# Kernel optimization log

Hardware: AMD Instinct MI355X
Metric: run time of the kernel (lower is better)

## Reference

```python
import jax, jax.numpy as jnp
import numpy as np

ND, NG, E = 25000, 20000, 1_000_000
DIN_D, DIN_G, H, OUT = 128, 128, 128, 128


def setup_inputs() -> dict:
    key = jax.random.key(0)
    ks = jax.random.split(key, 12)

    def w(k, i, o):
        return jax.random.normal(k, (i, o), jnp.float32) / np.float32(np.sqrt(i))

    return {
        "x_disease": jax.random.normal(ks[0], (ND, DIN_D), jnp.float32),
        "x_gene": jax.random.normal(ks[1], (NG, DIN_G), jnp.float32),
        "src": jax.random.randint(ks[2], (E,), 0, ND, dtype=jnp.int32),  # disease endpoint
        "dst": jax.random.randint(ks[3], (E,), 0, NG, dtype=jnp.int32),  # gene endpoint
        # layer 1, relation disease->gene: lin_l acts on aggregated disease feats, lin_r on gene feats
        "w1_dg_l": w(ks[4], DIN_D, H), "b1_dg": jnp.zeros((H,), jnp.float32), "w1_dg_r": w(ks[5], DIN_G, H),
        # layer 1, relation gene->disease (reverse edges)
        "w1_gd_l": w(ks[6], DIN_G, H), "b1_gd": jnp.zeros((H,), jnp.float32), "w1_gd_r": w(ks[7], DIN_D, H),
        # layer 2
        "w2_dg_l": w(ks[8], H, OUT), "b2_dg": jnp.zeros((OUT,), jnp.float32), "w2_dg_r": w(ks[9], H, OUT),
        "w2_gd_l": w(ks[10], H, OUT), "b2_gd": jnp.zeros((OUT,), jnp.float32), "w2_gd_r": w(ks[11], H, OUT),
    }


def _sage(x_src, x_dst, e_src, e_dst, n_dst, W_l, b_l, W_r):
    """Bipartite SAGEConv: lin_l(mean of source neighbors) + lin_r(x_dst)."""
    msg = x_src[e_src]                                         # [E, d] gather
    s = jax.ops.segment_sum(msg, e_dst, num_segments=n_dst)    # [n_dst, d]
    cnt = jax.ops.segment_sum(jnp.ones((e_dst.shape[0],), x_src.dtype),
                              e_dst, num_segments=n_dst)
    mean = s / jnp.maximum(cnt, 1.0)[:, None]                  # isolated nodes -> 0
    return mean @ W_l + b_l + x_dst @ W_r


def reference(x_disease, x_gene, src, dst,
              w1_dg_l, b1_dg, w1_dg_r, w1_gd_l, b1_gd, w1_gd_r,
              w2_dg_l, b2_dg, w2_dg_r, w2_gd_l, b2_gd, w2_gd_r):
    # HeteroConv aggr='sum': each node type receives from exactly one relation here,
    # so the cross-relation sum is the single relation output.
    g1 = _sage(x_disease, x_gene, src, dst, NG, w1_dg_l, b1_dg, w1_dg_r)   # gene <- disease
    d1 = _sage(x_gene, x_disease, dst, src, ND, w1_gd_l, b1_gd, w1_gd_r)   # disease <- gene (rev)
    g2 = _sage(d1, g1, src, dst, NG, w2_dg_l, b2_dg, w2_dg_r)
    d2 = _sage(g1, d1, dst, src, ND, w2_gd_l, b2_gd, w2_gd_r)
    return d2, g2
```

## Files before the change

### kernel.cpp

```cpp
#include <hip/hip_runtime.h>
#include <hip/hip_fp16.h>

#define ND 25000
#define NG 20000
#define NTOT (ND + NG)
#define NSCAN_BLOCKS 44
#define NBLK 128

typedef _Float16 half8 __attribute__((ext_vector_type(8)));
typedef float f32x4 __attribute__((ext_vector_type(4)));
typedef float f32x2 __attribute__((ext_vector_type(2)));

#define OFF_CNT    0ull
#define OFF_ROW    180224ull
#define OFF_BSUM   360448ull
#define OFF_PARTD  360704ull
#define OFF_PARTG  6760704ull
#define OFF_COL    11880704ull
#define OFF_WSW    15880704ull
#define OFF_XDH    16142848ull
#define OFF_XGH    22542848ull
#define OFF_X8D    27662848ull
#define OFF_X8G    30862848ull
#define OFF_MDH    33422848ull
#define OFF_MGH    39822848ull
#define OFF_D1H    44942848ull
#define OFF_G1H    51342848ull
#define OFF_D18    56462848ull
#define OFF_G18    59662848ull

struct WPtrs { const float* w[8]; };

__global__ __launch_bounds__(256) void prep(const float* __restrict__ xd,
                                            const float* __restrict__ xg,
                                            __half* __restrict__ yd,
                                            __half* __restrict__ yg,
                                            unsigned char* __restrict__ y8d,
                                            unsigned char* __restrict__ y8g,
                                            WPtrs p, _Float16* __restrict__ wsw) {
    int t = threadIdx.x;
    if (blockIdx.x < 8) {
        int mat = blockIdx.x;
        const float* W = p.w[mat];
        _Float16* o = wsw + (size_t)mat * 16384;
        for (int rep = 0; rep < 8; ++rep) {
            int slot = rep * 256 + t;
            int lane = slot & 63, grp = slot >> 6;
            int kc = grp & 3, ntile = grp >> 2;
            int nn = ntile * 16 + (lane & 15);
            int kb = kc * 32 + (lane >> 4) * 8;
            half8 v;
#pragma unroll
            for (int j = 0; j < 8; ++j) v[j] = (_Float16)W[(size_t)(kb + j) * 128 + nn];
            *(half8*)(o + (size_t)slot * 8) = v;
        }
        return;
    }
    const int ndq = ND * 32;
    const int tot = ndq + NG * 32;
    int i = (blockIdx.x - 8) * 256 + t;
    if (i >= tot) return;
    const float* x;
    __half* y;
    unsigned char* y8;
    int idx;
    if (i < ndq) { x = xd; y = yd; y8 = y8d; idx = i; }
    else         { x = xg; y = yg; y8 = y8g; idx = i - ndq; }
    float4 v = ((const float4*)x)[idx];
    ((__half2*)y)[idx * 2 + 0] = __floats2half2_rn(v.x, v.y);
    ((__half2*)y)[idx * 2 + 1] = __floats2half2_rn(v.z, v.w);
    int p8 = __builtin_amdgcn_cvt_pk_fp8_f32(v.x, v.y, 0, false);
    p8 = __builtin_amdgcn_cvt_pk_fp8_f32(v.z, v.w, p8, true);
    ((int*)y8)[idx] = p8;
}

__global__ __launch_bounds__(256) void hist2(const int* __restrict__ src,
                                             const int* __restrict__ dst,
                                             unsigned short* __restrict__ partD,
                                             unsigned short* __restrict__ partG, int E) {
    __shared__ unsigned int h[12544];
    int t = threadIdx.x, b = blockIdx.x;
    bool isD = b < NBLK;
    int bb = isD ? b : b - NBLK;
    const int* key = isD ? src : dst;
    int nw = isD ? (ND / 2) : (NG / 2);
    for (int i = t; i < nw; i += 256) h[i] = 0;
    __syncthreads();
    int e0 = (int)(((long long)E * bb) / NBLK);
    int e1 = (int)(((long long)E * (bb + 1)) / NBLK);
    for (int e = e0 + t; e < e1; e += 256) {
        int k = key[e];
        atomicAdd(&h[k >> 1], 1u << ((k & 1) * 16));
    }
    __syncthreads();
    unsigned int* po = (unsigned int*)((isD ? partD : partG) + (size_t)bb * (isD ? ND : NG));
    for (int i = t; i < nw; i += 256) po[i] = h[i];
}

__global__ __launch_bounds__(256) void colscan2(unsigned short* __restrict__ partD,
                                                unsigned short* __restrict__ partG,
                                                int* __restrict__ cnt) {
    int k = blockIdx.x * 256 + threadIdx.x;
    if (k >= NTOT) return;
    unsigned short* part;
    int nb, kk;
    if (k < ND) { part = partD; nb = ND; kk = k; }
    else        { part = partG; nb = NG; kk = k - ND; }
    int run = 0;
#pragma unroll 8
    for (int b = 0; b < NBLK; ++b) {
        size_t idx = (size_t)b * nb + kk;
        int v = part[idx];
        part[idx] = (unsigned short)run;
        run += v;
    }
    cnt[k] = run;
}

__global__ __launch_bounds__(256) void scan1(const int* __restrict__ cnt,
                                             int* __restrict__ row,
                                             int* __restrict__ bsum, int N) {
    __shared__ int sd[256];
    int t = threadIdx.x;
    int base = blockIdx.x * 1024 + t * 4;
    int v[4];
#pragma unroll
    for (int j = 0; j < 4; ++j) {
        int idx = base + j;
        v[j] = (idx < N) ? cnt[idx] : 0;
    }
    int tsum = v[0] + v[1] + v[2] + v[3];
    sd[t] = tsum;
    __syncthreads();
    for (int off = 1; off < 256; off <<= 1) {
        int x = (t >= off) ? sd[t - off] : 0;
        __syncthreads();
        sd[t] += x;
        __syncthreads();
    }
    int run = sd[t] - tsum;
#pragma unroll
    for (int j = 0; j < 4; ++j) {
        int idx = base + j;
        if (idx < N) row[idx] = run;
        run += v[j];
    }
    if (t == 255) bsum[blockIdx.x] = sd[255];
}

__global__ __launch_bounds__(256) void scan2(int* __restrict__ row,
                                             const int* __restrict__ bsum,
                                             int N, int total) {
    int off = 0;
    for (int b2 = 0; b2 < (int)blockIdx.x; ++b2) off += bsum[b2];
    int t = threadIdx.x;
    int base = blockIdx.x * 1024 + t * 4;
#pragma unroll
    for (int j = 0; j < 4; ++j) {
        int idx = base + j;
        if (idx < N) row[idx] += off;
    }
    if (blockIdx.x == 0 && t == 0) row[N] = total;
}

__global__ __launch_bounds__(256) void fill2(const int* __restrict__ src,
                                             const int* __restrict__ dst,
                                             const int* __restrict__ row,
                                             const unsigned short* __restrict__ partD,
                                             const unsigned short* __restrict__ partG,
                                             unsigned short* __restrict__ col, int E) {
    __shared__ unsigned int h[12544];
    int t = threadIdx.x, b = blockIdx.x;
    bool isD = b < NBLK;
    int bb = isD ? b : b - NBLK;
    const int* key = isD ? src : dst;
    const int* val = isD ? dst : src;
    const int* rowp = isD ? row : row + ND;
    int nw = isD ? (ND / 2) : (NG / 2);
    const unsigned int* pi =
        (const unsigned int*)((isD ? partD : partG) + (size_t)bb * (isD ? ND : NG));
    for (int i = t; i < nw; i += 256) h[i] = pi[i];
    __syncthreads();
    int e0 = (int)(((long long)E * bb) / NBLK);
    int e1 = (int)(((long long)E * (bb + 1)) / NBLK);
    for (int e = e0 + t; e < e1; e += 256) {
        int k = key[e];
        int v = val[e];
        unsigned int old = atomicAdd(&h[k >> 1], 1u << ((k & 1) * 16));
        int rank = (old >> ((k & 1) * 16)) & 0xffff;
        col[rowp[k] + rank] = (unsigned short)v;
    }
}

__global__ __launch_bounds__(256) void agg8m(const unsigned char* __restrict__ Xg,
                                             const unsigned char* __restrict__ Xd,
                                             const int* __restrict__ row,
                                             const unsigned short* __restrict__ col,
                                             __half* __restrict__ outd,
                                             __half* __restrict__ outg) {
    int wid = threadIdx.x >> 6, lane = threadIdx.x & 63;
    int node = blockIdx.x * 4 + wid;
    if (node >= NTOT) return;
    const unsigned char* X;
    _Float16* out;
    int nloc;
    if (node < ND) { X = Xg; out = (_Float16*)outd; nloc = node; }
    else           { X = Xd; out = (_Float16*)outg; nloc = node - ND; }
    int b = row[node], e = row[node + 1];
    int g = lane >> 3, f = lane & 7;
    float acc[16];
#pragma unroll
    for (int k = 0; k < 16; ++k) acc[k] = 0.f;
    int j = b + g;
    for (; j + 8 < e; j += 16) {
        int c0 = col[j], c1 = col[j + 8];
        int4 w0 = *(const int4*)(X + (size_t)c0 * 128 + f * 16);
        int4 w1 = *(const int4*)(X + (size_t)c1 * 128 + f * 16);
        const int* wa = (const int*)&w0;
        const int* wb = (const int*)&w1;
#pragma unroll
        for (int q = 0; q < 4; ++q) {
            f32x2 l0 = __builtin_amdgcn_cvt_pk_f32_fp8(wa[q], false);
            f32x2 h0 = __builtin_amdgcn_cvt_pk_f32_fp8(wa[q], true);
            f32x2 l1 = __builtin_amdgcn_cvt_pk_f32_fp8(wb[q], false);
            f32x2 h1 = __builtin_amdgcn_cvt_pk_f32_fp8(wb[q], true);
            acc[q * 4 + 0] += l0[0] + l1[0];
            acc[q * 4 + 1] += l0[1] + l1[1];
            acc[q * 4 + 2] += h0[0] + h1[0];
            acc[q * 4 + 3] += h0[1] + h1[1];
        }
    }
    if (j < e) {
        int c = col[j];
        int4 w = *(const int4*)(X + (size_t)c * 128 + f * 16);
        const int* wa = (const int*)&w;
#pragma unroll
        for (int q = 0; q < 4; ++q) {
            f32x2 l = __builtin_amdgcn_cvt_pk_f32_fp8(wa[q], false);
            f32x2 h = __builtin_amdgcn_cvt_pk_f32_fp8(wa[q], true);
            acc[q * 4 + 0] += l[0];
            acc[q * 4 + 1] += l[1];
            acc[q * 4 + 2] += h[0];
            acc[q * 4 + 3] += h[1];
        }
    }
#pragma unroll
    for (int k = 0; k < 16; ++k) {
        acc[k] += __shfl_xor(acc[k], 8, 64);
        acc[k] += __shfl_xor(acc[k], 16, 64);
        acc[k] += __shfl_xor(acc[k], 32, 64);
    }
    if (g == 0) {
        int deg = e - b;
        float r = 1.0f / (float)(deg > 0 ? deg : 1);
        half8 o0, o1;
#pragma unroll
        for (int k = 0; k < 8; ++k) o0[k] = (_Float16)(acc[k] * r);
#pragma unroll
        for (int k = 0; k < 8; ++k) o1[k] = (_Float16)(acc[8 + k] * r);
        _Float16* op = out + (size_t)nloc * 128 + f * 16;
        *(half8*)op = o0;
        *(half8*)(op + 8) = o1;
    }
}

struct GemmDual {
    const __half *A1d, *A2d, *A1g, *A2g;
    const _Float16 *W1d, *W2d, *W1g, *W2g;
    const float *biasd, *biasg;
    float *Yfd, *Yfg;
    __half *Yhd, *Yhg;
    unsigned char *Y8d, *Y8g;
};
__global__ __launch_bounds__(256) void gemm2(GemmDual p, int nblkD) {
    int bx = blockIdx.x;
    const __half *A1, *A2;
    const _Float16 *W1, *W2;
    const float* bias;
    float* Yf;
    __half* Yh;
    unsigned char* Y8;
    int n, b0;
    if (bx < nblkD) {
        A1 = p.A1d; A2 = p.A2d; W1 = p.W1d; W2 = p.W2d; bias = p.biasd;
        Yf = p.Yfd; Yh = p.Yhd; Y8 = p.Y8d; n = ND; b0 = bx;
    } else {
        A1 = p.A1g; A2 = p.A2g; W1 = p.W1g; W2 = p.W2g; bias = p.biasg;
        Yf = p.Yfg; Yh = p.Yhg; Y8 = p.Y8g; n = NG; b0 = bx - nblkD;
    }
    int t = threadIdx.x;
    int wave = t >> 6, lane = t & 63;
    int row0 = b0 * 64 + wave * 16;
    if (row0 >= n) return;
    int m = lane & 15, quad = lane >> 4;
    int arow = row0 + m;
    if (arow >= n) arow = n - 1;
    const _Float16* a1p = (const _Float16*)A1 + (size_t)arow * 128 + quad * 8;
    const _Float16* a2p = (const _Float16*)A2 + (size_t)arow * 128 + quad * 8;
    half8 a1[4], a2[4];
#pragma unroll
    for (int kc = 0; kc < 4; ++kc) {
        a1[kc] = *(const half8*)(a1p + kc * 32);
        a2[kc] = *(const half8*)(a2p + kc * 32);
    }
#pragma unroll
    for (int ntile = 0; ntile < 8; ++ntile) {
        f32x4 acc = {0.f, 0.f, 0.f, 0.f};
#pragma unroll
        for (int kc = 0; kc < 4; ++kc) {
            half8 b1 = *(const half8*)(W1 + (size_t)((ntile * 4 + kc) * 64 + lane) * 8);
            acc = __builtin_amdgcn_mfma_f32_16x16x32_f16(a1[kc], b1, acc, 0, 0, 0);
            half8 b2 = *(const half8*)(W2 + (size_t)((ntile * 4 + kc) * 64 + lane) * 8);
            acc = __builtin_amdgcn_mfma_f32_16x16x32_f16(a2[kc], b2, acc, 0, 0, 0);
        }
        int colx = ntile * 16 + m;
        float bb = bias[colx];
#pragma unroll
        for (int r = 0; r < 4; ++r) {
            int rr = row0 + quad * 4 + r;
            if (rr < n) {
                float v = acc[r] + bb;
                if (Yf) {
                    Yf[(size_t)rr * 128 + colx] = v;
                } else {
                    Yh[(size_t)rr * 128 + colx] = __float2half(v);
                    int p8 = __builtin_amdgcn_cvt_pk_fp8_f32(v, v, 0, false);
                    Y8[(size_t)rr * 128 + colx] = (unsigned char)(p8 & 0xff);
                }
            }
        }
    }
}

extern "C" void kernel_launch(void* const* d_in, const int* in_sizes, int n_in,
                              void* d_out, int out_size, void* d_ws, size_t ws_size,
                              hipStream_t stream) {
    const float* x_d     = (const float*)d_in[0];
    const float* x_g     = (const float*)d_in[1];
    const int*   src     = (const int*)d_in[2];
    const int*   dst     = (const int*)d_in[3];
    const float* w1_dg_l = (const float*)d_in[4];
    const float* b1_dg   = (const float*)d_in[5];
    const float* w1_dg_r = (const float*)d_in[6];
    const float* w1_gd_l = (const float*)d_in[7];
    const float* b1_gd   = (const float*)d_in[8];
    const float* w1_gd_r = (const float*)d_in[9];
    const float* w2_dg_l = (const float*)d_in[10];
    const float* b2_dg   = (const float*)d_in[11];
    const float* w2_dg_r = (const float*)d_in[12];
    const float* w2_gd_l = (const float*)d_in[13];
    const float* b2_gd   = (const float*)d_in[14];
    const float* w2_gd_r = (const float*)d_in[15];
    float* out = (float*)d_out;

    char* ws = (char*)d_ws;
    int*            cnt   = (int*)(ws + OFF_CNT);
    int*            row   = (int*)(ws + OFF_ROW);
    int*            bsum  = (int*)(ws + OFF_BSUM);
    unsigned short* partD = (unsigned short*)(ws + OFF_PARTD);
    unsigned short* partG = (unsigned short*)(ws + OFF_PARTG);
    unsigned short* col   = (unsigned short*)(ws + OFF_COL);
    _Float16*       wsw   = (_Float16*)(ws + OFF_WSW);
    __half*         xd_h  = (__half*)(ws + OFF_XDH);
    __half*         xg_h  = (__half*)(ws + OFF_XGH);
    unsigned char*  x8d   = (unsigned char*)(ws + OFF_X8D);
    unsigned char*  x8g   = (unsigned char*)(ws + OFF_X8G);
    __half*         md_h  = (__half*)(ws + OFF_MDH);
    __half*         mg_h  = (__half*)(ws + OFF_MGH);
    __half*         d1_h  = (__half*)(ws + OFF_D1H);
    __half*         g1_h  = (__half*)(ws + OFF_G1H);
    unsigned char*  d1_8  = (unsigned char*)(ws + OFF_D18);
    unsigned char*  g1_8  = (unsigned char*)(ws + OFF_G18);

    const int E = in_sizes[2];
    const int nblkD = (ND + 63) / 64;
    const int nblkG = (NG + 63) / 64;

    WPtrs wp;
    wp.w[0] = w1_dg_l; wp.w[1] = w1_dg_r; wp.w[2] = w1_gd_l; wp.w[3] = w1_gd_r;
    wp.w[4] = w2_dg_l; wp.w[5] = w2_dg_r; wp.w[6] = w2_gd_l; wp.w[7] = w2_gd_r;
    prep<<<8 + (NTOT * 32 + 255) / 256, 256, 0, stream>>>(x_d, x_g, xd_h, xg_h, x8d, x8g, wp, wsw);

    hist2<<<2 * NBLK, 256, 0, stream>>>(src, dst, partD, partG, E);
    colscan2<<<(NTOT + 255) / 256, 256, 0, stream>>>(partD, partG, cnt);
    scan1<<<NSCAN_BLOCKS, 256, 0, stream>>>(cnt, row, bsum, NTOT);
    scan2<<<NSCAN_BLOCKS, 256, 0, stream>>>(row, bsum, NTOT, 2 * E);
    fill2<<<2 * NBLK, 256, 0, stream>>>(src, dst, row, partD, partG, col, E);

    agg8m<<<(NTOT + 3) / 4, 256, 0, stream>>>(x8g, x8d, row, col, md_h, mg_h);
    GemmDual g1p;
    g1p.A1d = md_h; g1p.A2d = xd_h; g1p.W1d = wsw + 2 * 16384; g1p.W2d = wsw + 3 * 16384;
    g1p.biasd = b1_gd; g1p.Yfd = nullptr; g1p.Yhd = d1_h; g1p.Y8d = d1_8;
    g1p.A1g = mg_h; g1p.A2g = xg_h; g1p.W1g = wsw + 0 * 16384; g1p.W2g = wsw + 1 * 16384;
    g1p.biasg = b1_dg; g1p.Yfg = nullptr; g1p.Yhg = g1_h; g1p.Y8g = g1_8;
    gemm2<<<nblkD + nblkG, 256, 0, stream>>>(g1p, nblkD);

    agg8m<<<(NTOT + 3) / 4, 256, 0, stream>>>(g1_8, d1_8, row, col, md_h, mg_h);
    GemmDual g2p;
    g2p.A1d = md_h; g2p.A2d = d1_h; g2p.W1d = wsw + 6 * 16384; g2p.W2d = wsw + 7 * 16384;
    g2p.biasd = b2_gd; g2p.Yfd = out; g2p.Yhd = nullptr; g2p.Y8d = nullptr;
    g2p.A1g = mg_h; g2p.A2g = g1_h; g2p.W1g = wsw + 4 * 16384; g2p.W2g = wsw + 5 * 16384;
    g2p.biasg = b2_dg; g2p.Yfg = out + (size_t)ND * 128; g2p.Yhg = nullptr; g2p.Y8g = nullptr;
    gemm2<<<nblkD + nblkG, 256, 0, stream>>>(g2p, nblkD);
}
```

Before: 255.7 us.

## Fuse aggregation into GEMM via LDS, merge prep with histogram, single-block scan

Mean aggregation now runs inside the GEMM kernel. Each wave gathers and averages 16 node rows into LDS, then feeds them straight into the MFMA, so the fp16 mean buffers are no longer written to and re-read from global memory. Weight/feature prep and the edge histogram share one launch. The two-pass scan becomes a single 1024-thread block. Launches and global traffic drop, but each GEMM block now serializes 16 gathers per wave, and there are far fewer waves in flight for hiding gather latency.

```diff
diff --git a/kernel.cpp b/kernel.cpp
--- a/kernel.cpp
+++ b/kernel.cpp
@@ -4,8 +4,9 @@
 #define ND 25000
 #define NG 20000
 #define NTOT (ND + NG)
-#define NSCAN_BLOCKS 44
 #define NBLK 128
+#define PREPB 1024
+#define LDP 136
 
 typedef _Float16 half8 __attribute__((ext_vector_type(8)));
 typedef float f32x4 __attribute__((ext_vector_type(4)));
@@ -13,7 +14,6 @@
 
 #define OFF_CNT    0ull
 #define OFF_ROW    180224ull
-#define OFF_BSUM   360448ull
 #define OFF_PARTD  360704ull
 #define OFF_PARTG  6760704ull
 #define OFF_COL    11880704ull
@@ -22,27 +22,48 @@
 #define OFF_XGH    22542848ull
 #define OFF_X8D    27662848ull
 #define OFF_X8G    30862848ull
-#define OFF_MDH    33422848ull
-#define OFF_MGH    39822848ull
-#define OFF_D1H    44942848ull
-#define OFF_G1H    51342848ull
-#define OFF_D18    56462848ull
-#define OFF_G18    59662848ull
+#define OFF_D1H    33422848ull
+#define OFF_G1H    39822848ull
+#define OFF_D18    44942848ull
+#define OFF_G18    48142848ull
 
 struct WPtrs { const float* w[8]; };
 
-__global__ __launch_bounds__(256) void prep(const float* __restrict__ xd,
-                                            const float* __restrict__ xg,
-                                            __half* __restrict__ yd,
-                                            __half* __restrict__ yg,
-                                            unsigned char* __restrict__ y8d,
-                                            unsigned char* __restrict__ y8g,
-                                            WPtrs p, _Float16* __restrict__ wsw) {
-    int t = threadIdx.x;
-    if (blockIdx.x < 8) {
-        int mat = blockIdx.x;
-        const float* W = p.w[mat];
-        _Float16* o = wsw + (size_t)mat * 16384;
+__global__ __launch_bounds__(256) void prep_hist(const float* __restrict__ xd,
+                                                 const float* __restrict__ xg,
+                                                 __half* __restrict__ ydh,
+                                                 __half* __restrict__ ygh,
+                                                 unsigned char* __restrict__ y8d,
+                                                 unsigned char* __restrict__ y8g,
+                                                 WPtrs wp, _Float16* __restrict__ wsw,
+                                                 const int* __restrict__ src,
+                                                 const int* __restrict__ dst,
+                                                 unsigned short* __restrict__ partD,
+                                                 unsigned short* __restrict__ partG, int E) {
+    __shared__ unsigned int h[12544];
+    int bx = blockIdx.x, t = threadIdx.x;
+    if (bx < 2 * NBLK) {
+        bool isD = bx < NBLK;
+        int bb = isD ? bx : bx - NBLK;
+        const int* key = isD ? src : dst;
+        int nw = isD ? (ND / 2) : (NG / 2);
+        for (int i = t; i < nw; i += 256) h[i] = 0;
+        __syncthreads();
+        int e0 = (int)(((long long)E * bb) / NBLK);
+        int e1 = (int)(((long long)E * (bb + 1)) / NBLK);
+        for (int e = e0 + t; e < e1; e += 256) {
+            int k = key[e];
+            atomicAdd(&h[k >> 1], 1u << ((k & 1) * 16));
+        }
+        __syncthreads();
+        unsigned int* po = (unsigned int*)((isD ? partD : partG) + (size_t)bb * (isD ? ND : NG));
+        for (int i = t; i < nw; i += 256) po[i] = h[i];
+        return;
+    }
+    int pb = bx - 2 * NBLK;
+    if (pb < 8) {
+        const float* W = wp.w[pb];
+        _Float16* o = wsw + (size_t)pb * 16384;
         for (int rep = 0; rep < 8; ++rep) {
             int slot = rep * 256 + t;
             int lane = slot & 63, grp = slot >> 6;
@@ -54,47 +75,23 @@
             for (int j = 0; j < 8; ++j) v[j] = (_Float16)W[(size_t)(kb + j) * 128 + nn];
             *(half8*)(o + (size_t)slot * 8) = v;
         }
-        return;
     }
     const int ndq = ND * 32;
     const int tot = ndq + NG * 32;
-    int i = (blockIdx.x - 8) * 256 + t;
-    if (i >= tot) return;
-    const float* x;
-    __half* y;
-    unsigned char* y8;
-    int idx;
-    if (i < ndq) { x = xd; y = yd; y8 = y8d; idx = i; }
-    else         { x = xg; y = yg; y8 = y8g; idx = i - ndq; }
-    float4 v = ((const float4*)x)[idx];
-    ((__half2*)y)[idx * 2 + 0] = __floats2half2_rn(v.x, v.y);
-    ((__half2*)y)[idx * 2 + 1] = __floats2half2_rn(v.z, v.w);
-    int p8 = __builtin_amdgcn_cvt_pk_fp8_f32(v.x, v.y, 0, false);
-    p8 = __builtin_amdgcn_cvt_pk_fp8_f32(v.z, v.w, p8, true);
-    ((int*)y8)[idx] = p8;
-}
-
-__global__ __launch_bounds__(256) void hist2(const int* __restrict__ src,
-                                             const int* __restrict__ dst,
-                                             unsigned short* __restrict__ partD,
-                                             unsigned short* __restrict__ partG, int E) {
-    __shared__ unsigned int h[12544];
-    int t = threadIdx.x, b = blockIdx.x;
-    bool isD = b < NBLK;
-    int bb = isD ? b : b - NBLK;
-    const int* key = isD ? src : dst;
-    int nw = isD ? (ND / 2) : (NG / 2);
-    for (int i = t; i < nw; i += 256) h[i] = 0;
-    __syncthreads();
-    int e0 = (int)(((long long)E * bb) / NBLK);
-    int e1 = (int)(((long long)E * (bb + 1)) / NBLK);
-    for (int e = e0 + t; e < e1; e += 256) {
-        int k = key[e];
-        atomicAdd(&h[k >> 1], 1u << ((k & 1) * 16));
-    }
-    __syncthreads();
-    unsigned int* po = (unsigned int*)((isD ? partD : partG) + (size_t)bb * (isD ? ND : NG));
-    for (int i = t; i < nw; i += 256) po[i] = h[i];
+    for (int i = pb * 256 + t; i < tot; i += PREPB * 256) {
+        const float* x;
+        __half* y;
+        unsigned char* y8;
+        int idx;
+        if (i < ndq) { x = xd; y = ydh; y8 = y8d; idx = i; }
+        else         { x = xg; y = ygh; y8 = y8g; idx = i - ndq; }
+        float4 v = ((const float4*)x)[idx];
+        ((__half2*)y)[idx * 2 + 0] = __floats2half2_rn(v.x, v.y);
+        ((__half2*)y)[idx * 2 + 1] = __floats2half2_rn(v.z, v.w);
+        int p8 = __builtin_amdgcn_cvt_pk_fp8_f32(v.x, v.y, 0, false);
+        p8 = __builtin_amdgcn_cvt_pk_fp8_f32(v.z, v.w, p8, true);
+        ((int*)y8)[idx] = p8;
+    }
 }
 
 __global__ __launch_bounds__(256) void colscan2(unsigned short* __restrict__ partD,
@@ -117,50 +114,34 @@
     cnt[k] = run;
 }
 
-__global__ __launch_bounds__(256) void scan1(const int* __restrict__ cnt,
-                                             int* __restrict__ row,
-                                             int* __restrict__ bsum, int N) {
-    __shared__ int sd[256];
+__global__ __launch_bounds__(1024) void scanrow(const int* __restrict__ cnt,
+                                                int* __restrict__ row, int total) {
+    __shared__ int sd[1024];
     int t = threadIdx.x;
-    int base = blockIdx.x * 1024 + t * 4;
-    int v[4];
-#pragma unroll
-    for (int j = 0; j < 4; ++j) {
+    const int C = 44;
+    int base = t * C;
+    int sum = 0;
+    for (int j = 0; j < C; ++j) {
         int idx = base + j;
-        v[j] = (idx < N) ? cnt[idx] : 0;
-    }
-    int tsum = v[0] + v[1] + v[2] + v[3];
-    sd[t] = tsum;
+        if (idx < NTOT) sum += cnt[idx];
+    }
+    sd[t] = sum;
     __syncthreads();
-    for (int off = 1; off < 256; off <<= 1) {
+    for (int off = 1; off < 1024; off <<= 1) {
         int x = (t >= off) ? sd[t - off] : 0;
         __syncthreads();
         sd[t] += x;
         __syncthreads();
     }
-    int run = sd[t] - tsum;
-#pragma unroll
-    for (int j = 0; j < 4; ++j) {
+    int run = sd[t] - sum;
+    for (int j = 0; j < C; ++j) {
         int idx = base + j;
-        if (idx < N) row[idx] = run;
-        run += v[j];
-    }
-    if (t == 255) bsum[blockIdx.x] = sd[255];
-}
-
-__global__ __launch_bounds__(256) void scan2(int* __restrict__ row,
-                                             const int* __restrict__ bsum,
-                                             int N, int total) {
-    int off = 0;
-    for (int b2 = 0; b2 < (int)blockIdx.x; ++b2) off += bsum[b2];
-    int t = threadIdx.x;
-    int base = blockIdx.x * 1024 + t * 4;
-#pragma unroll
-    for (int j = 0; j < 4; ++j) {
-        int idx = base + j;
-        if (idx < N) row[idx] += off;
-    }
-    if (blockIdx.x == 0 && t == 0) row[N] = total;
+        if (idx < NTOT) {
+            row[idx] = run;
+            run += cnt[idx];
+        }
+    }
+    if (t == 1023) row[NTOT] = total;
 }
 
 __global__ __launch_bounds__(256) void fill2(const int* __restrict__ src,
@@ -192,115 +173,103 @@
     }
 }
 
-__global__ __launch_bounds__(256) void agg8m(const unsigned char* __restrict__ Xg,
-                                             const unsigned char* __restrict__ Xd,
-                                             const int* __restrict__ row,
-                                             const unsigned short* __restrict__ col,
-                                             __half* __restrict__ outd,
-                                             __half* __restrict__ outg) {
-    int wid = threadIdx.x >> 6, lane = threadIdx.x & 63;
-    int node = blockIdx.x * 4 + wid;
-    if (node >= NTOT) return;
-    const unsigned char* X;
-    _Float16* out;
-    int nloc;
-    if (node < ND) { X = Xg; out = (_Float16*)outd; nloc = node; }
-    else           { X = Xd; out = (_Float16*)outg; nloc = node - ND; }
-    int b = row[node], e = row[node + 1];
-    int g = lane >> 3, f = lane & 7;
-    float acc[16];
-#pragma unroll
-    for (int k = 0; k < 16; ++k) acc[k] = 0.f;
-    int j = b + g;
-    for (; j + 8 < e; j += 16) {
-        int c0 = col[j], c1 = col[j + 8];
-        int4 w0 = *(const int4*)(X + (size_t)c0 * 128 + f * 16);
-        int4 w1 = *(const int4*)(X + (size_t)c1 * 128 + f * 16);
-        const int* wa = (const int*)&w0;
-        const int* wb = (const int*)&w1;
-#pragma unroll
-        for (int q = 0; q < 4; ++q) {
-            f32x2 l0 = __builtin_amdgcn_cvt_pk_f32_fp8(wa[q], false);
-            f32x2 h0 = __builtin_amdgcn_cvt_pk_f32_fp8(wa[q], true);
-            f32x2 l1 = __builtin_amdgcn_cvt_pk_f32_fp8(wb[q], false);
-            f32x2 h1 = __builtin_amdgcn_cvt_pk_f32_fp8(wb[q], true);
-            acc[q * 4 + 0] += l0[0] + l1[0];
-            acc[q * 4 + 1] += l0[1] + l1[1];
-            acc[q * 4 + 2] += h0[0] + h1[0];
-            acc[q * 4 + 3] += h0[1] + h1[1];
-        }
-    }
-    if (j < e) {
-        int c = col[j];
-        int4 w = *(const int4*)(X + (size_t)c * 128 + f * 16);
-        const int* wa = (const int*)&w;
-#pragma unroll
-        for (int q = 0; q < 4; ++q) {
-            f32x2 l = __builtin_amdgcn_cvt_pk_f32_fp8(wa[q], false);
-            f32x2 h = __builtin_amdgcn_cvt_pk_f32_fp8(wa[q], true);
-            acc[q * 4 + 0] += l[0];
-            acc[q * 4 + 1] += l[1];
-            acc[q * 4 + 2] += h[0];
-            acc[q * 4 + 3] += h[1];
-        }
-    }
-#pragma unroll
-    for (int k = 0; k < 16; ++k) {
-        acc[k] += __shfl_xor(acc[k], 8, 64);
-        acc[k] += __shfl_xor(acc[k], 16, 64);
-        acc[k] += __shfl_xor(acc[k], 32, 64);
-    }
-    if (g == 0) {
-        int deg = e - b;
-        float r = 1.0f / (float)(deg > 0 ? deg : 1);
-        half8 o0, o1;
-#pragma unroll
-        for (int k = 0; k < 8; ++k) o0[k] = (_Float16)(acc[k] * r);
-#pragma unroll
-        for (int k = 0; k < 8; ++k) o1[k] = (_Float16)(acc[8 + k] * r);
-        _Float16* op = out + (size_t)nloc * 128 + f * 16;
-        *(half8*)op = o0;
-        *(half8*)(op + 8) = o1;
-    }
-}
-
-struct GemmDual {
-    const __half *A1d, *A2d, *A1g, *A2g;
+struct AG {
+    const unsigned char *Xg8, *Xd8;
+    const __half *A2d, *A2g;
     const _Float16 *W1d, *W2d, *W1g, *W2g;
     const float *biasd, *biasg;
-    float *Yfd, *Yfg;
+    const int* row;
+    const unsigned short* col;
     __half *Yhd, *Yhg;
     unsigned char *Y8d, *Y8g;
+    float *Yfd, *Yfg;
 };
-__global__ __launch_bounds__(256) void gemm2(GemmDual p, int nblkD) {
-    int bx = blockIdx.x;
-    const __half *A1, *A2;
-    const _Float16 *W1, *W2;
-    const float* bias;
-    float* Yf;
-    __half* Yh;
-    unsigned char* Y8;
-    int n, b0;
-    if (bx < nblkD) {
-        A1 = p.A1d; A2 = p.A2d; W1 = p.W1d; W2 = p.W2d; bias = p.biasd;
-        Yf = p.Yfd; Yh = p.Yhd; Y8 = p.Y8d; n = ND; b0 = bx;
-    } else {
-        A1 = p.A1g; A2 = p.A2g; W1 = p.W1g; W2 = p.W2g; bias = p.biasg;
-        Yf = p.Yfg; Yh = p.Yhg; Y8 = p.Y8g; n = NG; b0 = bx - nblkD;
-    }
-    int t = threadIdx.x;
+__global__ __launch_bounds__(256) void aggemm(AG p, int layer) {
+    __shared__ _Float16 am[4 * 16 * LDP];
+    const int nblkD = (ND + 63) / 64;
+    int bx = blockIdx.x, t = threadIdx.x;
+    bool isD = bx < nblkD;
+    int n = isD ? ND : NG, b0 = isD ? bx : bx - nblkD;
+    const unsigned char* X8 = isD ? p.Xg8 : p.Xd8;
+    const __half* A2 = isD ? p.A2d : p.A2g;
+    const _Float16* W1 = isD ? p.W1d : p.W1g;
+    const _Float16* W2 = isD ? p.W2d : p.W2g;
+    const float* bias = isD ? p.biasd : p.biasg;
+    const int* rowp = isD ? p.row : p.row + ND;
     int wave = t >> 6, lane = t & 63;
     int row0 = b0 * 64 + wave * 16;
     if (row0 >= n) return;
+    int g = lane >> 3, f = lane & 7;
+    _Float16* wbase = am + wave * 16 * LDP;
+
+    for (int i = 0; i < 16; ++i) {
+        int node = row0 + i;
+        int b = 0, e = 0;
+        if (node < n) { b = rowp[node]; e = rowp[node + 1]; }
+        float acc[16];
+#pragma unroll
+        for (int k = 0; k < 16; ++k) acc[k] = 0.f;
+        int j = b + g;
+        for (; j + 8 < e; j += 16) {
+            int c0 = p.col[j], c1 = p.col[j + 8];
+            int4 w0 = *(const int4*)(X8 + (size_t)c0 * 128 + f * 16);
+            int4 w1 = *(const int4*)(X8 + (size_t)c1 * 128 + f * 16);
+            const int* wa = (const int*)&w0;
+            const int* wb = (const int*)&w1;
+#pragma unroll
+            for (int q = 0; q < 4; ++q) {
+                f32x2 l0 = __builtin_amdgcn_cvt_pk_f32_fp8(wa[q], false);
+                f32x2 h0 = __builtin_amdgcn_cvt_pk_f32_fp8(wa[q], true);
+                f32x2 l1 = __builtin_amdgcn_cvt_pk_f32_fp8(wb[q], false);
+                f32x2 h1 = __builtin_amdgcn_cvt_pk_f32_fp8(wb[q], true);
+                acc[q * 4 + 0] += l0[0] + l1[0];
+                acc[q * 4 + 1] += l0[1] + l1[1];
+                acc[q * 4 + 2] += h0[0] + h1[0];
+                acc[q * 4 + 3] += h0[1] + h1[1];
+            }
+        }
+        if (j < e) {
+            int c = p.col[j];
+            int4 w = *(const int4*)(X8 + (size_t)c * 128 + f * 16);
+            const int* wa = (const int*)&w;
+#pragma unroll
+            for (int q = 0; q < 4; ++q) {
+                f32x2 l = __builtin_amdgcn_cvt_pk_f32_fp8(wa[q], false);
+                f32x2 h = __builtin_amdgcn_cvt_pk_f32_fp8(wa[q], true);
+                acc[q * 4 + 0] += l[0];
+                acc[q * 4 + 1] += l[1];
+                acc[q * 4 + 2] += h[0];
+                acc[q * 4 + 3] += h[1];
+            }
+        }
+#pragma unroll
+        for (int k = 0; k < 16; ++k) {
+            acc[k] += __shfl_xor(acc[k], 8, 64);
+            acc[k] += __shfl_xor(acc[k], 16, 64);
+            acc[k] += __shfl_xor(acc[k], 32, 64);
+        }
+        if (g == 0) {
+            int deg = e - b;
+            float r = 1.0f / (float)(deg > 0 ? deg : 1);
+            half8 o0, o1;
+#pragma unroll
+            for (int k = 0; k < 8; ++k) o0[k] = (_Float16)(acc[k] * r);
+#pragma unroll
+            for (int k = 0; k < 8; ++k) o1[k] = (_Float16)(acc[8 + k] * r);
+            _Float16* op = wbase + i * LDP + f * 16;
+            *(half8*)op = o0;
+            *(half8*)(op + 8) = o1;
+        }
+    }
+
     int m = lane & 15, quad = lane >> 4;
     int arow = row0 + m;
     if (arow >= n) arow = n - 1;
-    const _Float16* a1p = (const _Float16*)A1 + (size_t)arow * 128 + quad * 8;
     const _Float16* a2p = (const _Float16*)A2 + (size_t)arow * 128 + quad * 8;
     half8 a1[4], a2[4];
 #pragma unroll
     for (int kc = 0; kc < 4; ++kc) {
-        a1[kc] = *(const half8*)(a1p + kc * 32);
+        a1[kc] = *(const half8*)(wbase + m * LDP + kc * 32 + quad * 8);
         a2[kc] = *(const half8*)(a2p + kc * 32);
     }
 #pragma unroll
@@ -315,12 +284,15 @@
         }
         int colx = ntile * 16 + m;
         float bb = bias[colx];
+        float* Yf = isD ? p.Yfd : p.Yfg;
+        __half* Yh = isD ? p.Yhd : p.Yhg;
+        unsigned char* Y8 = isD ? p.Y8d : p.Y8g;
 #pragma unroll
         for (int r = 0; r < 4; ++r) {
             int rr = row0 + quad * 4 + r;
             if (rr < n) {
                 float v = acc[r] + bb;
-                if (Yf) {
+                if (layer == 2) {
                     Yf[(size_t)rr * 128 + colx] = v;
                 } else {
                     Yh[(size_t)rr * 128 + colx] = __float2half(v);
@@ -335,28 +307,15 @@
 extern "C" void kernel_launch(void* const* d_in, const int* in_sizes, int n_in,
                               void* d_out, int out_size, void* d_ws, size_t ws_size,
                               hipStream_t stream) {
-    const float* x_d     = (const float*)d_in[0];
-    const float* x_g     = (const float*)d_in[1];
-    const int*   src     = (const int*)d_in[2];
-    const int*   dst     = (const int*)d_in[3];
-    const float* w1_dg_l = (const float*)d_in[4];
-    const float* b1_dg   = (const float*)d_in[5];
-    const float* w1_dg_r = (const float*)d_in[6];
-    const float* w1_gd_l = (const float*)d_in[7];
-    const float* b1_gd   = (const float*)d_in[8];
-    const float* w1_gd_r = (const float*)d_in[9];
-    const float* w2_dg_l = (const float*)d_in[10];
-    const float* b2_dg   = (const float*)d_in[11];
-    const float* w2_dg_r = (const float*)d_in[12];
-    const float* w2_gd_l = (const float*)d_in[13];
-    const float* b2_gd   = (const float*)d_in[14];
-    const float* w2_gd_r = (const float*)d_in[15];
+    const float* x_d = (const float*)d_in[0];
+    const float* x_g = (const float*)d_in[1];
+    const int*   src = (const int*)d_in[2];
+    const int*   dst = (const int*)d_in[3];
     float* out = (float*)d_out;
 
     char* ws = (char*)d_ws;
     int*            cnt   = (int*)(ws + OFF_CNT);
     int*            row   = (int*)(ws + OFF_ROW);
-    int*            bsum  = (int*)(ws + OFF_BSUM);
     unsigned short* partD = (unsigned short*)(ws + OFF_PARTD);
     unsigned short* partG = (unsigned short*)(ws + OFF_PARTG);
     unsigned short* col   = (unsigned short*)(ws + OFF_COL);
@@ -365,8 +324,6 @@
     __half*         xg_h  = (__half*)(ws + OFF_XGH);
     unsigned char*  x8d   = (unsigned char*)(ws + OFF_X8D);
     unsigned char*  x8g   = (unsigned char*)(ws + OFF_X8G);
-    __half*         md_h  = (__half*)(ws + OFF_MDH);
-    __half*         mg_h  = (__half*)(ws + OFF_MGH);
     __half*         d1_h  = (__half*)(ws + OFF_D1H);
     __half*         g1_h  = (__half*)(ws + OFF_G1H);
     unsigned char*  d1_8  = (unsigned char*)(ws + OFF_D18);
@@ -377,29 +334,44 @@
     const int nblkG = (NG + 63) / 64;
 
     WPtrs wp;
-    wp.w[0] = w1_dg_l; wp.w[1] = w1_dg_r; wp.w[2] = w1_gd_l; wp.w[3] = w1_gd_r;
-    wp.w[4] = w2_dg_l; wp.w[5] = w2_dg_r; wp.w[6] = w2_gd_l; wp.w[7] = w2_gd_r;
-    prep<<<8 + (NTOT * 32 + 255) / 256, 256, 0, stream>>>(x_d, x_g, xd_h, xg_h, x8d, x8g, wp, wsw);
-
-    hist2<<<2 * NBLK, 256, 0, stream>>>(src, dst, partD, partG, E);
+    wp.w[0] = (const float*)d_in[4];
+    wp.w[1] = (const float*)d_in[6];
+    wp.w[2] = (const float*)d_in[7];
+    wp.w[3] = (const float*)d_in[9];
+    wp.w[4] = (const float*)d_in[10];
+    wp.w[5] = (const float*)d_in[12];
+    wp.w[6] = (const float*)d_in[13];
+    wp.w[7] = (const float*)d_in[15];
+    const float* b1_dg = (const float*)d_in[5];
+    const float* b1_gd = (const float*)d_in[8];
+    const float* b2_dg = (const float*)d_in[11];
+    const float* b2_gd = (const float*)d_in[14];
+
+    prep_hist<<<2 * NBLK + PREPB, 256, 0, stream>>>(x_d, x_g, xd_h, xg_h, x8d, x8g,
+                                                    wp, wsw, src, dst, partD, partG, E);
     colscan2<<<(NTOT + 255) / 256, 256, 0, stream>>>(partD, partG, cnt);
-    scan1<<<NSCAN_BLOCKS, 256, 0, stream>>>(cnt, row, bsum, NTOT);
-    scan2<<<NSCAN_BLOCKS, 256, 0, stream>>>(row, bsum, NTOT, 2 * E);
+    scanrow<<<1, 1024, 0, stream>>>(cnt, row, 2 * E);
     fill2<<<2 * NBLK, 256, 0, stream>>>(src, dst, row, partD, partG, col, E);
 
-    agg8m<<<(NTOT + 3) / 4, 256, 0, stream>>>(x8g, x8d, row, col, md_h, mg_h);
-    GemmDual g1p;
-    g1p.A1d = md_h; g1p.A2d = xd_h; g1p.W1d = wsw + 2 * 16384; g1p.W2d = wsw + 3 * 16384;
-    g1p.biasd = b1_gd; g1p.Yfd = nullptr; g1p.Yhd = d1_h; g1p.Y8d = d1_8;
-    g1p.A1g = mg_h; g1p.A2g = xg_h; g1p.W1g = wsw + 0 * 16384; g1p.W2g = wsw + 1 * 16384;
-    g1p.biasg = b1_dg; g1p.Yfg = nullptr; g1p.Yhg = g1_h; g1p.Y8g = g1_8;
-    gemm2<<<nblkD + nblkG, 256, 0, stream>>>(g1p, nblkD);
-
-    agg8m<<<(NTOT + 3) / 4, 256, 0, stream>>>(g1_8, d1_8, row, col, md_h, mg_h);
-    GemmDual g2p;
-    g2p.A1d = md_h; g2p.A2d = d1_h; g2p.W1d = wsw + 6 * 16384; g2p.W2d = wsw + 7 * 16384;
-    g2p.biasd = b2_gd; g2p.Yfd = out; g2p.Yhd = nullptr; g2p.Y8d = nullptr;
-    g2p.A1g = mg_h; g2p.A2g = g1_h; g2p.W1g = wsw + 4 * 16384; g2p.W2g = wsw + 5 * 16384;
-    g2p.biasg = b2_dg; g2p.Yfg = out + (size_t)ND * 128; g2p.Yhg = nullptr; g2p.Y8g = nullptr;
-    gemm2<<<nblkD + nblkG, 256, 0, stream>>>(g2p, nblkD);
-}
+    AG a1;
+    a1.Xg8 = x8g; a1.Xd8 = x8d;
+    a1.A2d = xd_h; a1.A2g = xg_h;
+    a1.W1d = wsw + 2 * 16384; a1.W2d = wsw + 3 * 16384;
+    a1.W1g = wsw + 0 * 16384; a1.W2g = wsw + 1 * 16384;
+    a1.biasd = b1_gd; a1.biasg = b1_dg;
+    a1.row = row; a1.col = col;
+    a1.Yhd = d1_h; a1.Yhg = g1_h; a1.Y8d = d1_8; a1.Y8g = g1_8;
+    a1.Yfd = nullptr; a1.Yfg = nullptr;
+    aggemm<<<nblkD + nblkG, 256, 0, stream>>>(a1, 1);
+
+    AG a2;
+    a2.Xg8 = g1_8; a2.Xd8 = d1_8;
+    a2.A2d = d1_h; a2.A2g = g1_h;
+    a2.W1d = wsw + 6 * 16384; a2.W2d = wsw + 7 * 16384;
+    a2.W1g = wsw + 4 * 16384; a2.W2g = wsw + 5 * 16384;
+    a2.biasd = b2_gd; a2.biasg = b2_dg;
+    a2.row = row; a2.col = col;
+    a2.Yhd = nullptr; a2.Yhg = nullptr; a2.Y8d = nullptr; a2.Y8g = nullptr;
+    a2.Yfd = out; a2.Yfg = out + (size_t)ND * 128;
+    aggemm<<<nblkD + nblkG, 256, 0, stream>>>(a2, 2);
+}
```

Result: slower. 372.7 us (+45.8%).
